# Kernel tuning notes

Hardware: AMD Instinct MI355X
Metric: run time of the kernel (lower is better)

Reference implementation:

```python
import jax, jax.numpy as jnp
import numpy as np

N = 20000          # nodes
E = 640000         # edges (avg in-degree 32)
H = 8              # attention heads
CK = 32            # key/query channels per degree
CV = 32            # value channels per degree
DK = 16            # per-head key dim = (32*1 + 32*3)/8
KEY_FEATS = 128    # key_fiber.num_features = 32*1 + 32*3
DV = 4             # fused value degree dim = 1 + 3


def setup_inputs() -> dict:
    key = jax.random.key(0)
    k1, k2, k3, k4, k5 = jax.random.split(key, 5)
    return {
        "key": jax.random.normal(k1, (E, H, DK), dtype=jnp.float32),
        "query_0": jax.random.normal(k2, (N, CK, 1), dtype=jnp.float32),
        "query_1": jax.random.normal(k3, (N, CK, 3), dtype=jnp.float32),
        "value": jax.random.normal(k4, (E, CV, DV), dtype=jnp.float32),
        "edge_dst": jnp.sort(jax.random.randint(k5, (E,), 0, N, dtype=jnp.int32)),
    }


def reference(key, query_0, query_1, value, edge_dst):
    # fuse query degrees and split into heads: (N, C, 1+3) -> (N, H, DK)
    q = jnp.concatenate([query_0, query_1], axis=-1).reshape(N, H, DK)
    # e_dot_v: per-edge dot product with destination-node query -> (E, H)
    ew = jnp.einsum('ehd,ehd->eh', key, q[edge_dst]) / np.float32(np.sqrt(KEY_FEATS))
    # edge_softmax grouped by destination node (numerically stable)
    m = jax.ops.segment_max(ew, edge_dst, num_segments=N, indices_are_sorted=True)
    ex = jnp.exp(ew - m[edge_dst])
    den = jax.ops.segment_sum(ex, edge_dst, num_segments=N, indices_are_sorted=True)
    w = ex / den[edge_dst]                       # (E, H)
    # weighted sum of multi-degree values, scattered to destination nodes
    v = value.reshape(E, H, CV // H, DV)         # (E, H, C/H, DV)
    weighted = (w[:, :, None, None] * v).reshape(E, H * (CV // H) * DV)
    feat = jax.ops.segment_sum(weighted, edge_dst, num_segments=N,
                               indices_are_sorted=True).reshape(N, CV, DV)
    # unfuse_features: split last dim by degree dims (1, 3)
    return feat[..., :1], feat[..., 1:]
```

## Files before the change

### kernel.cpp

```cpp
#include <hip/hip_runtime.h>
#include <math.h>

#define NN 20000
#define EE 640000

__global__ __launch_bounds__(128)
void attn_se3_kernel(const float* __restrict__ key,
                     const float* __restrict__ q0,
                     const float* __restrict__ q1,
                     const float* __restrict__ val,
                     const int*   __restrict__ dst,
                     float*       __restrict__ out)
{
    const int n = blockIdx.x;
    const int t = threadIdx.x;
    const int c  = t >> 2;
    const int dv = t & 3;

    float q;
    if (dv == 0) q = q0[n * 32 + c];
    else         q = q1[n * 96 + c * 3 + (dv - 1)];

    int lo = 0, hi = EE;
    while (lo < hi) { int mid = (lo + hi) >> 1; if (dst[mid] <  n) lo = mid + 1; else hi = mid; }
    const int start = lo;
    hi = EE;
    while (lo < hi) { int mid = (lo + hi) >> 1; if (dst[mid] <= n) lo = mid + 1; else hi = mid; }
    const int end = lo;

    float r = 0.0f;
    if (start < end) {
        const float scale = 0.08838834764831845f;
        float m = -INFINITY, l = 0.0f, acc = 0.0f;

        float kc = key[(long)start * 128 + t];
        float vc = val[(long)start * 128 + t];

        for (int e = start; e < end; ++e) {
            float kn = 0.0f, vn = 0.0f;
            if (e + 1 < end) {
                kn = key[(long)(e + 1) * 128 + t];
                vn = val[(long)(e + 1) * 128 + t];
            }
            float p = kc * q;
            p += __shfl_xor(p, 1);
            p += __shfl_xor(p, 2);
            p += __shfl_xor(p, 4);
            p += __shfl_xor(p, 8);
            const float s  = p * scale;
            const float nm = fmaxf(m, s);
            const float alpha = __expf(m - nm);
            const float w     = __expf(s - nm);
            l   = l   * alpha + w;
            acc = acc * alpha + w * vc;
            m = nm;
            kc = kn; vc = vn;
        }
        r = acc / l;
    }
    if (dv == 0) out[n * 32 + c] = r;
    else         out[NN * 32 + n * 96 + c * 3 + (dv - 1)] = r;
}

extern "C" void kernel_launch(void* const* d_in, const int* in_sizes, int n_in,
                              void* d_out, int out_size, void* d_ws, size_t ws_size,
                              hipStream_t stream) {
    const float* key = (const float*)d_in[0];
    const float* q0  = (const float*)d_in[1];
    const float* q1  = (const float*)d_in[2];
    const float* val = (const float*)d_in[3];
    const int*   dst = (const int*)d_in[4];
    float* out = (float*)d_out;

    attn_se3_kernel<<<NN, 128, 0, stream>>>(key, q0, q1, val, dst, out);
}
```

Measured before the change: 666.5 us.

## Precompute CSR offsets and process two edges per wave with float4 loads

Replaces the per-block binary search over edge_dst with a separate kernel that builds CSR row offsets in workspace. The attention kernel now maps one 64-lane wave to each node. Each half-wave handles alternating edges, with each lane loading a float4 of key and value, and the two partial online-softmax states are merged at the end. This reduces search overhead, widens memory accesses and doubles edge-level parallelism per node. The cost is an extra kernel launch, a dependence on workspace, and a merge step.

```diff
diff --git a/kernel.cpp b/kernel.cpp
--- a/kernel.cpp
+++ b/kernel.cpp
@@ -4,62 +4,106 @@
 #define NN 20000
 #define EE 640000
 
-__global__ __launch_bounds__(128)
+__global__ __launch_bounds__(256)
+void build_offsets(const int* __restrict__ dst, int* __restrict__ offs) {
+    int e = blockIdx.x * 256 + threadIdx.x;
+    if (e >= EE) return;
+    int d = dst[e];
+    if (e == 0) {
+        for (int j = 0; j <= d; ++j) offs[j] = 0;
+    } else {
+        int dp = dst[e - 1];
+        for (int j = dp + 1; j <= d; ++j) offs[j] = e;
+    }
+    if (e == EE - 1) {
+        for (int j = d + 1; j <= NN; ++j) offs[j] = EE;
+    }
+}
+
+__global__ __launch_bounds__(256)
 void attn_se3_kernel(const float* __restrict__ key,
                      const float* __restrict__ q0,
                      const float* __restrict__ q1,
                      const float* __restrict__ val,
-                     const int*   __restrict__ dst,
+                     const int*   __restrict__ offs,
                      float*       __restrict__ out)
 {
-    const int n = blockIdx.x;
-    const int t = threadIdx.x;
-    const int c  = t >> 2;
-    const int dv = t & 3;
+    const int wid  = threadIdx.x >> 6;
+    const int lane = threadIdx.x & 63;
+    const int n    = blockIdx.x * 4 + wid;
+    const int s    = lane >> 5;
+    const int cl   = lane & 31;
 
-    float q;
-    if (dv == 0) q = q0[n * 32 + c];
-    else         q = q1[n * 96 + c * 3 + (dv - 1)];
+    float4 qv;
+    qv.x = q0[n * 32 + cl];
+    qv.y = q1[n * 96 + cl * 3 + 0];
+    qv.z = q1[n * 96 + cl * 3 + 1];
+    qv.w = q1[n * 96 + cl * 3 + 2];
 
-    int lo = 0, hi = EE;
-    while (lo < hi) { int mid = (lo + hi) >> 1; if (dst[mid] <  n) lo = mid + 1; else hi = mid; }
-    const int start = lo;
-    hi = EE;
-    while (lo < hi) { int mid = (lo + hi) >> 1; if (dst[mid] <= n) lo = mid + 1; else hi = mid; }
-    const int end = lo;
+    const int start = offs[n];
+    const int end   = offs[n + 1];
+    const int deg   = end - start;
+    const int iters = (deg + 1) >> 1;
 
-    float r = 0.0f;
-    if (start < end) {
-        const float scale = 0.08838834764831845f;
-        float m = -INFINITY, l = 0.0f, acc = 0.0f;
+    const float scale = 0.08838834764831845f;
+    float m = -1e30f, l = 0.0f;
+    float4 acc = make_float4(0.f, 0.f, 0.f, 0.f);
 
-        float kc = key[(long)start * 128 + t];
-        float vc = val[(long)start * 128 + t];
+    int e = start + s;
+    float4 kc = make_float4(0.f, 0.f, 0.f, 0.f);
+    float4 vc = kc;
+    if (e < end) {
+        kc = *(const float4*)(key + (long)e * 128 + cl * 4);
+        vc = *(const float4*)(val + (long)e * 128 + cl * 4);
+    }
 
-        for (int e = start; e < end; ++e) {
-            float kn = 0.0f, vn = 0.0f;
-            if (e + 1 < end) {
-                kn = key[(long)(e + 1) * 128 + t];
-                vn = val[(long)(e + 1) * 128 + t];
-            }
-            float p = kc * q;
-            p += __shfl_xor(p, 1);
-            p += __shfl_xor(p, 2);
-            p += __shfl_xor(p, 4);
-            p += __shfl_xor(p, 8);
-            const float s  = p * scale;
-            const float nm = fmaxf(m, s);
-            const float alpha = __expf(m - nm);
-            const float w     = __expf(s - nm);
-            l   = l   * alpha + w;
-            acc = acc * alpha + w * vc;
-            m = nm;
-            kc = kn; vc = vn;
+    for (int i = 0; i < iters; ++i) {
+        const int en = e + 2;
+        float4 kn = make_float4(0.f, 0.f, 0.f, 0.f);
+        float4 vn = kn;
+        if (en < end) {
+            kn = *(const float4*)(key + (long)en * 128 + cl * 4);
+            vn = *(const float4*)(val + (long)en * 128 + cl * 4);
         }
-        r = acc / l;
+        const bool valid = (e < end);
+        float p = fmaf(kc.x, qv.x, fmaf(kc.y, qv.y, fmaf(kc.z, qv.z, kc.w * qv.w)));
+        p += __shfl_xor(p, 1);
+        p += __shfl_xor(p, 2);
+        const float sc = valid ? p * scale : -1e30f;
+        const float nm = fmaxf(m, sc);
+        const float al = __expf(m - nm);
+        const float w  = valid ? __expf(sc - nm) : 0.0f;
+        l = l * al + w;
+        acc.x = fmaf(w, vc.x, acc.x * al);
+        acc.y = fmaf(w, vc.y, acc.y * al);
+        acc.z = fmaf(w, vc.z, acc.z * al);
+        acc.w = fmaf(w, vc.w, acc.w * al);
+        m = nm;
+        kc = kn; vc = vn; e = en;
     }
-    if (dv == 0) out[n * 32 + c] = r;
-    else         out[NN * 32 + n * 96 + c * 3 + (dv - 1)] = r;
+
+    const float m2 = __shfl_xor(m, 32);
+    const float l2 = __shfl_xor(l, 32);
+    float4 a2;
+    a2.x = __shfl_xor(acc.x, 32);
+    a2.y = __shfl_xor(acc.y, 32);
+    a2.z = __shfl_xor(acc.z, 32);
+    a2.w = __shfl_xor(acc.w, 32);
+    const float mm = fmaxf(m, m2);
+    const float b1 = __expf(m - mm);
+    const float b2 = __expf(m2 - mm);
+    const float ll = l * b1 + l2 * b2;
+
+    if (lane < 32) {
+        const float inv = (ll > 0.f) ? 1.0f / ll : 0.0f;
+        const float rx = fmaf(acc.x, b1, a2.x * b2) * inv;
+        const float ry = fmaf(acc.y, b1, a2.y * b2) * inv;
+        const float rz = fmaf(acc.z, b1, a2.z * b2) * inv;
+        const float rw = fmaf(acc.w, b1, a2.w * b2) * inv;
+        out[n * 32 + cl] = rx;
+        float* o1 = out + NN * 32 + n * 96 + cl * 3;
+        o1[0] = ry; o1[1] = rz; o1[2] = rw;
+    }
 }
 
 extern "C" void kernel_launch(void* const* d_in, const int* in_sizes, int n_in,
@@ -71,6 +115,8 @@
     const float* val = (const float*)d_in[3];
     const int*   dst = (const int*)d_in[4];
     float* out = (float*)d_out;
+    int*   offs = (int*)d_ws;
 
-    attn_se3_kernel<<<NN, 128, 0, stream>>>(key, q0, q1, val, dst, out);
+    build_offsets<<<(EE + 255) / 256, 256, 0, stream>>>(dst, offs);
+    attn_se3_kernel<<<NN / 4, 256, 0, stream>>>(key, q0, q1, val, offs, out);
 }
```

Measured after the change: 631.7 us. -5.2%, faster.
